# Kernel tuning notes

Hardware: AMD Instinct MI355X
Metric: run time of the kernel (lower is better)

## Reference

```python
import jax, jax.numpy as jnp
import numpy as np

NP, NC, E, EL = 50000, 5000, 200000, 100000
DP, DC, HID, OUT, HEADS = 1280, 256, 128, 128, 4


def setup_inputs() -> dict:
    key = jax.random.key(0)
    ks = jax.random.split(key, 40)
    p = lambda k, shp: jax.random.normal(k, shp, dtype=jnp.float32) * 0.05
    inp = {
        "x_protein": jax.random.normal(ks[0], (NP, DP), dtype=jnp.float32),
        "x_class": jax.random.normal(ks[1], (NC, DC), dtype=jnp.float32),
        "src": jax.random.randint(ks[2], (E,), 0, NP),
        "dst": jax.random.randint(ks[3], (E,), 0, NC),
        "edge_label_src": jax.random.randint(ks[4], (EL,), 0, NP),
        "edge_label_dst": jax.random.randint(ks[5], (EL,), 0, NC),
        # SAGEConv, relation protein->class (updates class nodes)
        "sage_pc_Wl": p(ks[6], (DP, HID)), "sage_pc_bl": p(ks[7], (HID,)), "sage_pc_Wr": p(ks[8], (DC, HID)),
        # SAGEConv, relation class->protein (updates protein nodes)
        "sage_cp_Wl": p(ks[9], (DC, HID)), "sage_cp_bl": p(ks[10], (HID,)), "sage_cp_Wr": p(ks[11], (DP, HID)),
        # GATConv p->c (inputs are hidden after conv1)
        "gat_pc_Wsrc": p(ks[12], (HID, HEADS * HID)), "gat_pc_Wdst": p(ks[13], (HID, HEADS * HID)),
        "gat_pc_asrc": p(ks[14], (HEADS, HID)), "gat_pc_adst": p(ks[15], (HEADS, HID)), "gat_pc_b": p(ks[16], (HID,)),
        # GATConv c->p
        "gat_cp_Wsrc": p(ks[17], (HID, HEADS * HID)), "gat_cp_Wdst": p(ks[18], (HID, HEADS * HID)),
        "gat_cp_asrc": p(ks[19], (HEADS, HID)), "gat_cp_adst": p(ks[20], (HEADS, HID)), "gat_cp_b": p(ks[21], (HID,)),
        # final per-node-type Linear (to_hetero duplicates lin per node type)
        "lin_p_W": p(ks[22], (HID, OUT)), "lin_p_b": p(ks[23], (OUT,)),
        "lin_c_W": p(ks[24], (HID, OUT)), "lin_c_b": p(ks[25], (OUT,)),
        # link predictor
        "link_W": p(ks[26], (2 * OUT, 1)), "link_b": p(ks[27], (1,)),
    }
    return inp


def _sage(x_src, x_dst, s, d, Wl, bl, Wr, n_dst):
    # PyG SAGEConv: lin_l(mean_aggr(x_src)) + lin_r(x_dst); lin_l has bias.
    agg = jax.ops.segment_sum(x_src[s], d, num_segments=n_dst)
    cnt = jax.ops.segment_sum(jnp.ones((s.shape[0], 1), x_src.dtype), d, num_segments=n_dst)
    mean = agg / jnp.maximum(cnt, 1.0)
    return mean @ Wl + bl + x_dst @ Wr


def _gat(x_src, x_dst, s, d, Ws, Wd, a_s, a_d, b, n_dst):
    # PyG GATConv bipartite, heads=HEADS, concat=False, add_self_loops=False.
    H, C = a_s.shape
    hs = (x_src @ Ws).reshape(-1, H, C)   # [Ns, H, C]
    hd = (x_dst @ Wd).reshape(-1, H, C)   # [Nd, H, C]
    als = jnp.einsum('nhc,hc->nh', hs, a_s)
    ald = jnp.einsum('nhc,hc->nh', hd, a_d)
    e = jax.nn.leaky_relu(als[s] + ald[d], 0.2)                    # [E, H]
    emax = jax.ops.segment_max(e, d, num_segments=n_dst)          # stable softmax per dst
    ee = jnp.exp(e - emax[d])
    denom = jax.ops.segment_sum(ee, d, num_segments=n_dst)
    alpha = ee / denom[d]                                          # [E, H]
    out = jax.ops.segment_sum(alpha[:, :, None] * hs[s], d, num_segments=n_dst)  # [Nd, H, C]
    return out.mean(axis=1) + b  # concat=False -> mean over heads


def reference(x_protein, x_class, src, dst, edge_label_src, edge_label_dst,
              sage_pc_Wl, sage_pc_bl, sage_pc_Wr,
              sage_cp_Wl, sage_cp_bl, sage_cp_Wr,
              gat_pc_Wsrc, gat_pc_Wdst, gat_pc_asrc, gat_pc_adst, gat_pc_b,
              gat_cp_Wsrc, gat_cp_Wdst, gat_cp_asrc, gat_cp_adst, gat_cp_b,
              lin_p_W, lin_p_b, lin_c_W, lin_c_b, link_W, link_b):
    # Layer 1: hetero SAGE (each node type has exactly one incoming relation)
    h_c = jax.nn.relu(_sage(x_protein, x_class, src, dst, sage_pc_Wl, sage_pc_bl, sage_pc_Wr, NC))
    h_p = jax.nn.relu(_sage(x_class, x_protein, dst, src, sage_cp_Wl, sage_cp_bl, sage_cp_Wr, NP))
    # Layer 2: hetero GAT
    g_c = jax.nn.relu(_gat(h_p, h_c, src, dst, gat_pc_Wsrc, gat_pc_Wdst, gat_pc_asrc, gat_pc_adst, gat_pc_b, NC))
    g_p = jax.nn.relu(_gat(h_c, h_p, dst, src, gat_cp_Wsrc, gat_cp_Wdst, gat_cp_asrc, gat_cp_adst, gat_cp_b, NP))
    # Per-type output projection
    z_p = g_p @ lin_p_W + lin_p_b
    z_c = g_c @ lin_c_W + lin_c_b
    # Link predictor: gather, concat, linear, sigmoid
    ef = jnp.concatenate([z_p[edge_label_src], z_c[edge_label_dst]], axis=-1)  # [EL, 2*OUT]
    return jax.nn.sigmoid(ef @ link_W + link_b).squeeze(-1)
```

## Files before the change

kernel.cpp:

```cpp
#include <hip/hip_runtime.h>
#include <math.h>

#define NPROT 50000
#define NCLS  5000
#define DIMP  1280
#define DIMC  256
#define SCAN_N (NCLS + NPROT)
#define KSTEPS (DIMP/32)

#define P1B  ((NPROT+127)/128)
#define C1BY ((NCLS+63)/64)
#define C1B  (4*C1BY)

typedef float4 f4;
typedef __attribute__((ext_vector_type(8))) short short8;
typedef __attribute__((ext_vector_type(4))) float f32x4;

__device__ __forceinline__ unsigned short f2bf(float f){
    unsigned u = __float_as_uint(f);
    u += 0x7FFFu + ((u >> 16) & 1u);
    return (unsigned short)(u >> 16);
}
__device__ __forceinline__ float bf2f(unsigned short b){
    return __uint_as_float(((unsigned)b) << 16);
}
__device__ __forceinline__ void gload_lds16(const void* g, void* l){
    __builtin_amdgcn_global_load_lds((const __attribute__((address_space(1))) void*)g,
                                     (__attribute__((address_space(3))) void*)l, 16, 0, 0);
}
__device__ __forceinline__ int OFFV(const int* __restrict__ offv, const int* __restrict__ part, int v){
    return offv[v] + part[v>>10];
}

__global__ __launch_bounds__(512) void mega1(const float* __restrict__ Af,
                                             const unsigned short* __restrict__ BtP,
                                             unsigned short* __restrict__ P1,
                                             const float* __restrict__ Ac,
                                             const float* __restrict__ WcatC,
                                             unsigned short* __restrict__ C1,
                                             const int* __restrict__ src, const int* __restrict__ dst,
                                             const int* __restrict__ offv, const int* __restrict__ part,
                                             int* __restrict__ cur, int* __restrict__ adj, int E){
    __shared__ __align__(16) unsigned char smem[48*1024];
    const int blk = blockIdx.x;
    const int tid = threadIdx.x;

    if(blk < P1B){
        unsigned char* As = smem;
        unsigned char* Bs = smem + 16*1024;
        const int lane = tid & 63;
        const int w    = tid >> 6;
        const int wm   = w >> 2, wn = w & 3;
        const int row0 = blk * 128;
        const int kg = lane >> 4, fr = lane & 15;

        const int ar_  = tid >> 2;
        const int acc_ = tid & 3;
        const int asrow = min(row0 + ar_, NPROT-1);
        const float* aG = Af + (size_t)asrow*DIMP + acc_*8;
        const int awoff = ar_*64 + ((acc_ ^ ((ar_>>1)&3)) << 4);

        f32x4 acc[4][4] = {};
        f4 va, vb;

        auto STAGEB = [&](int buf, int k0){
            #pragma unroll
            for(int i=0;i<2;i++){
                int c  = i*512 + tid;
                int r  = c >> 2, cc = c & 3;
                int scc = cc ^ ((r>>1) & 3);
                gload_lds16((const void*)(BtP + (size_t)r*DIMP + k0 + scc*8),
                            (void*)(Bs + buf*16384 + (i*512 + tid)*16));
            }
        };
        auto WRITEA = [&](int buf){
            union { short8 s; unsigned short u[8]; } uu;
            uu.u[0]=f2bf(va.x); uu.u[1]=f2bf(va.y); uu.u[2]=f2bf(va.z); uu.u[3]=f2bf(va.w);
            uu.u[4]=f2bf(vb.x); uu.u[5]=f2bf(vb.y); uu.u[6]=f2bf(vb.z); uu.u[7]=f2bf(vb.w);
            *(short8*)(As + buf*8192 + awoff) = uu.s;
        };

        STAGEB(0, 0);
        va = *(const f4*)(aG + 0);
        vb = *(const f4*)(aG + 4);
        WRITEA(0);
        va = *(const f4*)(aG + 32);
        vb = *(const f4*)(aG + 36);
        asm volatile("s_waitcnt lgkmcnt(0)" ::: "memory");
        __builtin_amdgcn_sched_barrier(0);

        for(int t=0; t<KSTEPS; ++t){
            __builtin_amdgcn_s_barrier();
            __builtin_amdgcn_sched_barrier(0);

            if(t+1 < KSTEPS){
                WRITEA((t+1)&1);
                STAGEB((t+1)&1, (t+1)*32);
            }
            __builtin_amdgcn_sched_barrier(0);
            if(t+2 < KSTEPS){
                va = *(const f4*)(aG + (t+2)*32);
                vb = *(const f4*)(aG + (t+2)*32 + 4);
            }

            const unsigned char* Ab = As + (t&1)*8192;
            const unsigned char* Bb = Bs + (t&1)*16384;
            short8 aF[4], bF[4];
            #pragma unroll
            for(int m=0;m<4;m++){
                int r = wm*64 + m*16 + fr;
                aF[m] = *(const short8*)(Ab + r*64 + ((kg ^ ((r>>1)&3))<<4));
            }
            #pragma unroll
            for(int n=0;n<4;n++){
                int r = wn*64 + n*16 + fr;
                bF[n] = *(const short8*)(Bb + r*64 + ((kg ^ ((r>>1)&3))<<4));
            }
            #pragma unroll
            for(int m=0;m<4;m++)
            #pragma unroll
            for(int n=0;n<4;n++)
                acc[m][n] = __builtin_amdgcn_mfma_f32_16x16x32_bf16(aF[m], bF[n], acc[m][n], 0, 0, 0);

            if(t+2 < KSTEPS)      asm volatile("s_waitcnt vmcnt(2) lgkmcnt(0)" ::: "memory");
            else                  asm volatile("s_waitcnt vmcnt(0) lgkmcnt(0)" ::: "memory");
            __builtin_amdgcn_sched_barrier(0);
        }

        #pragma unroll
        for(int m=0;m<4;m++)
        #pragma unroll
        for(int r=0;r<4;r++){
            int row = row0 + wm*64 + m*16 + kg*4 + r;
            if(row < NPROT){
                #pragma unroll
                for(int n=0;n<4;n++)
                    P1[(size_t)row*256 + wn*64 + n*16 + fr] = f2bf(acc[m][n][r]);
            }
        }
    } else if(blk < P1B + C1B){
        float (*As64)[68] = (float(*)[68])smem;
        float (*Bs64)[64] = (float(*)[64])(smem + 16*68*4);
        const int bi = blk - P1B;
        const int row0 = (bi >> 2) * 64;
        const int col0 = (bi & 3) * 64;
        const bool act = tid < 256;
        const int ty = tid >> 4;
        const int tx = tid & 15;
        const int m  = tid >> 2;
        const int kq = (tid & 3) << 2;
        const int kb = tid >> 4;
        const int c4 = (tid & 15) << 2;

        float acc[4][4];
        #pragma unroll
        for(int i=0;i<4;i++)
        #pragma unroll
            for(int j=0;j<4;j++) acc[i][j]=0.f;

        const bool arow_ok = act && (row0 + m) < NCLS;
        const float* Abase = Ac + (size_t)(row0 + min(m,255)) * DIMC + kq;
        const float* Bbase = WcatC + col0 + c4 + (size_t)min(kb,15) * 256;

        for(int k0 = 0; k0 < DIMC; k0 += 16){
            if(act){
                f4 av;
                if(arow_ok) av = *(const f4*)(Abase + k0);
                else        av = make_float4(0.f,0.f,0.f,0.f);
                As64[kq+0][m]=av.x; As64[kq+1][m]=av.y; As64[kq+2][m]=av.z; As64[kq+3][m]=av.w;
                *(f4*)&Bs64[kb][c4] = *(const f4*)(Bbase + (size_t)k0 * 256);
            }
            __syncthreads();
            if(act){
                #pragma unroll
                for(int kk=0;kk<16;kk++){
                    f4 a = *(const f4*)&As64[kk][ty<<2];
                    f4 b = *(const f4*)&Bs64[kk][tx<<2];
                    float ar[4]={a.x,a.y,a.z,a.w};
                    float br[4]={b.x,b.y,b.z,b.w};
                    #pragma unroll
                    for(int i=0;i<4;i++)
                    #pragma unroll
                        for(int j=0;j<4;j++) acc[i][j] += ar[i]*br[j];
                }
            }
            __syncthreads();
        }
        if(act){
            #pragma unroll
            for(int i=0;i<4;i++){
                int r = row0 + (ty<<2) + i;
                if(r < NCLS){
                    ushort4 v;
                    v.x=f2bf(acc[i][0]); v.y=f2bf(acc[i][1]);
                    v.z=f2bf(acc[i][2]); v.w=f2bf(acc[i][3]);
                    *(ushort4*)&C1[(size_t)r*256 + col0 + (tx<<2)] = v;
                }
            }
        }
    } else {
        int e = (blk - P1B - C1B)*512 + tid;
        if(e < E){
            int s = src[e], d = dst[e];
            int pc = atomicAdd(&cur[d],1);        adj[OFFV(offv,part,d)+pc] = s;
            int pp = atomicAdd(&cur[NCLS+s],1);   adj[OFFV(offv,part,NCLS+s)+pp] = d;
        }
    }
}

#define NPB ((NPROT+127)/128)
#define NCB ((NCLS+127)/128)
__global__ __launch_bounds__(256) void gemm_hs(const unsigned short* __restrict__ Ap,
                                               const unsigned short* __restrict__ Ac,
                                               const unsigned short* __restrict__ Btp,
                                               const unsigned short* __restrict__ Btc,
                                               const float* __restrict__ projP,
                                               const float* __restrict__ projC,
                                               unsigned short* __restrict__ Cp,
                                               unsigned short* __restrict__ Cc,
                                               float* __restrict__ attP,
                                               float* __restrict__ attC){
    const bool cls = (int)blockIdx.y >= NPB;
    const unsigned short* A  = cls ? Ac : Ap;
    const unsigned short* Bt = cls ? Btc : Btp;
    unsigned short* C = cls ? Cc : Cp;
    const int M = cls ? NCLS : NPROT;
    const int row0 = (cls ? blockIdx.y - NPB : blockIdx.y) * 128;
    const int col0 = blockIdx.x * 128;

    __shared__ __align__(16) unsigned char As[128*32*2];
    __shared__ __align__(16) unsigned char Bs[128*32*2];
    __shared__ float projS[1024];
    const int tid  = threadIdx.x;
    const int lane = tid & 63;
    const int w    = tid >> 6;
    const int wm   = w >> 1, wn = w & 1;
    const int kg = lane >> 4, fr = lane & 15;

    f32x4 acc[4][4] = {};

    for(int k0 = 0; k0 < 128; k0 += 32){
        #pragma unroll
        for(int i=0;i<2;i++){
            int c  = i*256 + w*64 + lane;
            int r  = c >> 2, cc = c & 3;
            int scc = cc ^ ((r>>1) & 3);
            int srow = min(row0 + r, M-1);
            gload_lds16((const void*)(A + (size_t)srow*128 + k0 + scc*8),
                        (void*)(As + (i*256 + w*64)*16));
        }
        #pragma unroll
        for(int i=0;i<2;i++){
            int c  = i*256 + w*64 + lane;
            int r  = c >> 2, cc = c & 3;
            int scc = cc ^ ((r>>1) & 3);
            gload_lds16((const void*)(Bt + (size_t)(col0 + r)*128 + k0 + scc*8),
                        (void*)(Bs + (i*256 + w*64)*16));
        }
        __syncthreads();

        short8 aF[4], bF[4];
        #pragma unroll
        for(int m=0;m<4;m++){
            int r = wm*64 + m*16 + fr;
            int b0 = (r*64 + kg*16) ^ (((r>>1)&3)<<4);
            aF[m] = *(const short8*)(As + b0);
        }
        #pragma unroll
        for(int n=0;n<4;n++){
            int r = wn*64 + n*16 + fr;
            int b0 = (r*64 + kg*16) ^ (((r>>1)&3)<<4);
            bF[n] = *(const short8*)(Bs + b0);
        }
        #pragma unroll
        for(int m=0;m<4;m++)
        #pragma unroll
        for(int n=0;n<4;n++)
            acc[m][n] = __builtin_amdgcn_mfma_f32_16x16x32_bf16(aF[m], bF[n], acc[m][n], 0, 0, 0);
        __syncthreads();
    }

    #pragma unroll
    for(int m=0;m<4;m++)
    #pragma unroll
    for(int r=0;r<4;r++){
        int row = row0 + wm*64 + m*16 + kg*4 + r;
        if(row < M){
            #pragma unroll
            for(int n=0;n<4;n++)
                C[(size_t)row*512 + col0 + wn*64 + n*16 + fr] = f2bf(acc[m][n][r]);
        }
    }

    if(blockIdx.x == 0){
        const float* proj = cls ? projC : projP;
        float* att = cls ? attC : attP;
        for(int i=tid;i<1024;i+=256) projS[i] = proj[i];
        __syncthreads();
        int ri = tid >> 1, cb = (tid & 1)*4;
        int row = row0 + ri;
        if(row < M){
            const unsigned short* ar = A + (size_t)row*128;
            float s0=0.f,s1=0.f,s2=0.f,s3=0.f;
            #pragma unroll
            for(int kk=0;kk<16;kk++){
                short8 a8 = *(const short8*)(ar + kk*8);
                #pragma unroll
                for(int q=0;q<8;q++){
                    float av = bf2f((unsigned short)a8[q]);
                    const float* pr = &projS[(kk*8+q)*8 + cb];
                    s0 += av*pr[0]; s1 += av*pr[1]; s2 += av*pr[2]; s3 += av*pr[3];
                }
            }
            f4 o = make_float4(s0,s1,s2,s3);
            *(f4*)&att[(size_t)row*8 + cb] = o;
        }
    }
}

__global__ void setup(const float* __restrict__ Wl_pc, const float* __restrict__ Wr_cp,
                      const float* __restrict__ Wl_cp, const float* __restrict__ Wr_pc,
                      const float* __restrict__ pcWs, const float* __restrict__ pcAs,
                      const float* __restrict__ pcWd, const float* __restrict__ pcAd,
                      const float* __restrict__ cpWs, const float* __restrict__ cpAs,
                      const float* __restrict__ cpWd, const float* __restrict__ cpAd,
                      const float* __restrict__ lpW, const float* __restrict__ lpb,
                      const float* __restrict__ lcW, const float* __restrict__ lcb,
                      const float* __restrict__ linkW,
                      const int* __restrict__ src, const int* __restrict__ dst,
                      unsigned short* __restrict__ BtP, float* __restrict__ WcatC,
                      unsigned short* __restrict__ BtSp, unsigned short* __restrict__ BtSc,
                      float* __restrict__ projP, float* __restrict__ projC,
                      float* __restrict__ w_p, float* __restrict__ w_c,
                      float* __restrict__ cpc,
                      int* __restrict__ deg, int E){
    int blk = blockIdx.x, tid = threadIdx.x;
    if(blk < 2048){
        int t = blk*256 + tid;
        if(t < 327680){
            int n = t / 1280, k = t % 1280;
            float v = (n<128) ? Wl_pc[(size_t)k*128+n] : Wr_cp[(size_t)k*128+n-128];
            BtP[t] = f2bf(v);
        } else if(t < 393216){
            int i = t - 327680; int k = i>>8, j = i&255;
            WcatC[i] = (j<128) ? Wl_cp[(size_t)k*128+j] : Wr_pc[(size_t)k*128+j-128];
        } else if(t < 458752){
            int i = t - 393216; int n = i>>7, k = i&127;
            BtSp[i] = f2bf(pcWs[(size_t)k*512+n]);
        } else {
            int i = t - 458752; int n = i>>7, k = i&127;
            BtSc[i] = f2bf(cpWs[(size_t)k*512+n]);
        }
    } else if(blk < 2056){
        int sec = (blk-2048) >> 1;
        int t = ((blk-2048) & 1)*256 + tid;
        const float *W, *a; float* proj; int colbase;
        if(sec==0){ W=pcWs; a=pcAs; proj=projP; colbase=0; }
        else if(sec==1){ W=cpWd; a=cpAd; proj=projP; colbase=4; }
        else if(sec==2){ W=pcWd; a=pcAd; proj=projC; colbase=0; }
        else { W=cpWs; a=cpAs; proj=projC; colbase=4; }
        int k = t >> 2, h = t & 3;
        const float* w = W + (size_t)k*512 + h*128;
        const float* av = a + h*128;
        float s=0.f;
        for(int c=0;c<128;c++) s += w[c]*av[c];
        proj[k*8 + colbase + h] = s;
    } else if(blk == 2056){
        if(tid < 128){
            float s=0.f;
            for(int o=0;o<128;o++) s += lpW[(size_t)tid*128+o]*linkW[o];
            w_p[tid]=s;
        } else {
            int j=tid-128;
            float s=0.f;
            for(int o=0;o<128;o++) s += lcW[(size_t)j*128+o]*linkW[128+o];
            w_c[j]=s;
        }
        if(tid==0){ float s=0.f; for(int o=0;o<128;o++) s+=lpb[o]*linkW[o];      cpc[0]=s; }
        if(tid==1){ float s=0.f; for(int o=0;o<128;o++) s+=lcb[o]*linkW[128+o];  cpc[1]=s; }
    } else {
        int e = (blk-2057)*256 + tid;
        if(e < E){
            atomicAdd(&deg[dst[e]],1);
            atomicAdd(&deg[NCLS + src[e]],1);
        }
    }
}

__global__ __launch_bounds__(1024) void scan1(const int* __restrict__ in, int* __restrict__ out,
                                              int* __restrict__ part, int n){
    __shared__ int buf[1024];
    int tid = threadIdx.x;
    int g = blockIdx.x*1024 + tid;
    int v = (g<n) ? in[g] : 0;
    buf[tid] = v;
    __syncthreads();
    for(int o=1;o<1024;o<<=1){
        int t = (tid>=o) ? buf[tid-o] : 0;
        __syncthreads();
        buf[tid] += t;
        __syncthreads();
    }
    if(g<n) out[g] = buf[tid] - v;
    if(tid==1023) part[blockIdx.x] = buf[1023];
}
__global__ __launch_bounds__(64) void scan2(int* __restrict__ part, int nb,
                                            int* __restrict__ offv, int n){
    int tid = threadIdx.x;
    int orig = (tid<nb) ? part[tid] : 0;
    int v = orig;
    #pragma unroll
    for(int o=1;o<64;o<<=1){
        int t = __shfl_up(v, o);
        if(tid>=o) v += t;
    }
    int total = __shfl(v, nb-1);
    if(tid<nb) part[tid] = v - orig;
    if(tid == (n>>10)) offv[n] = total - (v - orig);
}

__global__ __launch_bounds__(256) void sage_all(const int* __restrict__ offv, const int* __restrict__ part,
                                                const int* __restrict__ adj,
                                                const unsigned short* __restrict__ P1,
                                                const unsigned short* __restrict__ C1,
                                                const float* __restrict__ bl_pc, const float* __restrict__ bl_cp,
                                                unsigned short* __restrict__ h_c, unsigned short* __restrict__ h_p){
    int v = blockIdx.x*4 + (threadIdx.x>>6);
    int l = threadIdx.x & 63;
    if(v >= SCAN_N) return;
    int b = OFFV(offv,part,v), deg = OFFV(offv,part,v+1)-b;
    float a0=0.f, a1=0.f;
    float inv = 1.f/(float)max(deg,1);
    if(v < NCLS){
        #pragma unroll 4
        for(int i=0;i<deg;i++){
            int s = adj[b+i];
            ushort2 w = *((const ushort2*)P1 + (size_t)s*128 + l);
            a0 += bf2f(w.x); a1 += bf2f(w.y);
        }
        ushort2 sv = *((const ushort2*)C1 + (size_t)v*128 + 64 + l);
        float h0 = fmaxf(a0*inv + bl_pc[2*l]   + bf2f(sv.x), 0.f);
        float h1 = fmaxf(a1*inv + bl_pc[2*l+1] + bf2f(sv.y), 0.f);
        ushort2 o; o.x=f2bf(h0); o.y=f2bf(h1);
        *((ushort2*)h_c + (size_t)v*64 + l) = o;
    } else {
        int m = v - NCLS;
        #pragma unroll 4
        for(int i=0;i<deg;i++){
            int d = adj[b+i];
            ushort2 w = *((const ushort2*)C1 + (size_t)d*128 + l);
            a0 += bf2f(w.x); a1 += bf2f(w.y);
        }
        ushort2 sv = *((const ushort2*)P1 + (size_t)m*128 + 64 + l);
        float h0 = fmaxf(a0*inv + bl_cp[2*l]   + bf2f(sv.x), 0.f);
        float h1 = fmaxf(a1*inv + bl_cp[2*l+1] + bf2f(sv.y), 0.f);
        ushort2 o; o.x=f2bf(h0); o.y=f2bf(h1);
        *((ushort2*)h_p + (size_t)m*64 + l) = o;
    }
}

__global__ __launch_bounds__(128) void gat_all(const int* __restrict__ offv, const int* __restrict__ part,
                                               const int* __restrict__ adj,
                                               const float* __restrict__ attP, const float* __restrict__ attC,
                                               const unsigned short* __restrict__ hs_p,
                                               const unsigned short* __restrict__ hs_c,
                                               const float* __restrict__ gb_pc, const float* __restrict__ gb_cp,
                                               const float* __restrict__ w_c, const float* __restrict__ w_p,
                                               const float* __restrict__ cpc,
                                               float* __restrict__ u_c, float* __restrict__ u_p){
    __shared__ float ald[4];
    __shared__ int   adjS[32];
    __shared__ float eeS[32*4];
    __shared__ float den8[8];
    __shared__ f4    red4[32];

    int n = blockIdx.x;
    const bool cls = n < NCLS;
    const int node = cls ? n : n - NCLS;
    const float* attS = cls ? attP : attC;
    const float* attD = cls ? attC : attP;
    const int abase = cls ? 0 : 4;
    const unsigned short* hs = cls ? hs_p : hs_c;
    const float* gb = cls ? gb_pc : gb_cp;
    const float* wv = cls ? w_c : w_p;
    float* u = cls ? u_c : u_p;
    const int cidx = cls ? 1 : 0;

    int j = threadIdx.x;
    const int hh = j >> 5;
    const int q  = j & 31;
    int b = OFFV(offv,part,n), deg = OFFV(offv,part,n+1)-b;
    if(j < 4) ald[j] = attD[(size_t)node*8 + abase + j];

    float a0=0.f, a1=0.f, a2=0.f, a3=0.f;
    float denP = 0.f;

    for(int base=0; base<deg; base+=32){
        int cnt = min(32, deg-base);
        if(j < cnt) adjS[j] = adj[b+base+j];
        __syncthreads();
        if(j < cnt*4){
            int i = j>>2, h = j&3;
            int s = adjS[i];
            float e = attS[(size_t)s*8 + abase + h] + ald[h];
            e = e > 0.f ? e : 0.2f*e;
            float ee = __expf(e);
            eeS[j] = ee;
            denP += ee;
        }
        __syncthreads();
        #pragma unroll 4
        for(int ii=0; ii<cnt; ii++){
            int s = adjS[ii];
            float ee = eeS[ii*4 + hh];
            ushort4 v = *(const ushort4*)(hs + (size_t)s*512 + hh*128 + q*4);
            a0 += ee*bf2f(v.x); a1 += ee*bf2f(v.y);
            a2 += ee*bf2f(v.z); a3 += ee*bf2f(v.w);
        }
        __syncthreads();
    }

    float dp = denP;
    dp += __shfl_xor(dp, 4);
    dp += __shfl_xor(dp, 8);
    dp += __shfl_xor(dp, 16);
    dp += __shfl_xor(dp, 32);
    if((j & 63) < 4) den8[(j>>6)*4 + (j&3)] = dp;
    __syncthreads();

    float den_h = den8[hh] + den8[4+hh];
    float inv = (deg > 0) ? 0.25f/den_h : 0.f;
    a0 *= inv; a1 *= inv; a2 *= inv; a3 *= inv;

    a0 += __shfl_xor(a0, 32); a1 += __shfl_xor(a1, 32);
    a2 += __shfl_xor(a2, 32); a3 += __shfl_xor(a3, 32);
    if(j >= 64 && j < 96) red4[q] = make_float4(a0,a1,a2,a3);
    __syncthreads();
    float val = 0.f;
    if(j < 32){
        f4 r = red4[q];
        float t0 = a0 + r.x, t1 = a1 + r.y, t2 = a2 + r.z, t3 = a3 + r.w;
        const float* gbq = gb + q*4;
        const float* wvq = wv + q*4;
        val = fmaxf(t0 + gbq[0], 0.f)*wvq[0]
            + fmaxf(t1 + gbq[1], 0.f)*wvq[1]
            + fmaxf(t2 + gbq[2], 0.f)*wvq[2]
            + fmaxf(t3 + gbq[3], 0.f)*wvq[3];
    }
    #pragma unroll
    for(int o=16;o;o>>=1) val += __shfl_down(val, o);
    if(j == 0) u[node] = val + cpc[cidx];
}

__global__ void link_out(const int* __restrict__ els, const int* __restrict__ eld,
                         const float* __restrict__ u_p, const float* __restrict__ u_c,
                         const float* __restrict__ linkb, float* __restrict__ out, int EL){
    int i = blockIdx.x*256 + threadIdx.x;
    if(i >= EL) return;
    float x = u_p[els[i]] + u_c[eld[i]] + linkb[0];
    out[i] = 1.f/(1.f + __expf(-x));
}

extern "C" void kernel_launch(void* const* d_in, const int* in_sizes, int n_in,
                              void* d_out, int out_size, void* d_ws, size_t ws_size,
                              hipStream_t stream){
    const float* x_p  = (const float*)d_in[0];
    const float* x_c  = (const float*)d_in[1];
    const int*   src  = (const int*)d_in[2];
    const int*   dst  = (const int*)d_in[3];
    const int*   els  = (const int*)d_in[4];
    const int*   eld  = (const int*)d_in[5];
    const float* sage_pc_Wl = (const float*)d_in[6];
    const float* sage_pc_bl = (const float*)d_in[7];
    const float* sage_pc_Wr = (const float*)d_in[8];
    const float* sage_cp_Wl = (const float*)d_in[9];
    const float* sage_cp_bl = (const float*)d_in[10];
    const float* sage_cp_Wr = (const float*)d_in[11];
    const float* gat_pc_Wsrc = (const float*)d_in[12];
    const float* gat_pc_Wdst = (const float*)d_in[13];
    const float* gat_pc_asrc = (const float*)d_in[14];
    const float* gat_pc_adst = (const float*)d_in[15];
    const float* gat_pc_b    = (const float*)d_in[16];
    const float* gat_cp_Wsrc = (const float*)d_in[17];
    const float* gat_cp_Wdst = (const float*)d_in[18];
    const float* gat_cp_asrc = (const float*)d_in[19];
    const float* gat_cp_adst = (const float*)d_in[20];
    const float* gat_cp_b    = (const float*)d_in[21];
    const float* lin_p_W = (const float*)d_in[22];
    const float* lin_p_b = (const float*)d_in[23];
    const float* lin_c_W = (const float*)d_in[24];
    const float* lin_c_b = (const float*)d_in[25];
    const float* link_W  = (const float*)d_in[26];
    const float* link_b  = (const float*)d_in[27];

    const int E  = in_sizes[2];
    const int EL = in_sizes[4];

    float* ws = (float*)d_ws;
    size_t off = 0;
    auto alloc = [&](size_t n)->float*{ float* p = ws + off; off += (n + 3) & ~(size_t)3; return p; };

    unsigned short* BtP  = (unsigned short*)alloc((size_t)256*DIMP/2);
    float* WcatC = alloc((size_t)DIMC*256);
    unsigned short* BtSp = (unsigned short*)alloc((size_t)512*128/2);
    unsigned short* BtSc = (unsigned short*)alloc((size_t)512*128/2);
    unsigned short* P1   = (unsigned short*)alloc((size_t)NPROT*256/2);
    unsigned short* C1   = (unsigned short*)alloc((size_t)NCLS*256/2);
    unsigned short* h_p  = (unsigned short*)alloc((size_t)NPROT*128/2);
    unsigned short* h_c  = (unsigned short*)alloc((size_t)NCLS*128/2);
    unsigned short* hs_p = (unsigned short*)alloc((size_t)NPROT*512/2);
    unsigned short* hs_c = (unsigned short*)alloc((size_t)NCLS*512/2);
    float* attP  = alloc((size_t)NPROT*8);
    float* attC  = alloc((size_t)NCLS*8);
    float* projP = alloc(128*8);
    float* projC = alloc(128*8);
    float* w_p   = alloc(128);
    float* w_c   = alloc(128);
    float* cpc   = alloc(4);
    int* degcur = (int*)alloc((size_t)2*SCAN_N);
    int* deg = degcur;
    int* cur = degcur + SCAN_N;
    int* offv = (int*)alloc(SCAN_N+1);
    int* part = (int*)alloc(64);
    int* adj  = (int*)alloc((size_t)2*E);
    float* u_p = alloc(NPROT);
    float* u_c = alloc(NCLS);
    if(off*4 > ws_size) return;

    hipMemsetAsync(degcur, 0, (size_t)2*SCAN_N*4, stream);

    setup<<<2057 + (E+255)/256, 256, 0, stream>>>(
        sage_pc_Wl, sage_cp_Wr, sage_cp_Wl, sage_pc_Wr,
        gat_pc_Wsrc, gat_pc_asrc, gat_pc_Wdst, gat_pc_adst,
        gat_cp_Wsrc, gat_cp_asrc, gat_cp_Wdst, gat_cp_adst,
        lin_p_W, lin_p_b, lin_c_W, lin_c_b, link_W,
        src, dst,
        BtP, WcatC, BtSp, BtSc, projP, projC, w_p, w_c, cpc, deg, E);

    const int NB = (SCAN_N + 1023)/1024;
    scan1<<<NB,1024,0,stream>>>(deg, offv, part, SCAN_N);
    scan2<<<1,64,0,stream>>>(part, NB, offv, SCAN_N);

    const int FILLB = (E+511)/512;
    mega1<<<P1B + C1B + FILLB, 512, 0, stream>>>(x_p, BtP, P1, x_c, WcatC, C1,
                                                 src, dst, offv, part, cur, adj, E);

    sage_all<<<(SCAN_N+3)/4,256,0,stream>>>(offv, part, adj, P1, C1, sage_pc_bl, sage_cp_bl, h_c, h_p);

    gemm_hs<<<dim3(4,NPB+NCB),256,0,stream>>>(h_p, h_c, BtSp, BtSc, projP, projC,
                                              hs_p, hs_c, attP, attC);

    gat_all<<<SCAN_N,128,0,stream>>>(offv, part, adj, attP, attC, hs_p, hs_c,
                                     gat_pc_b, gat_cp_b, w_c, w_p, cpc, u_c, u_p);

    link_out<<<(EL+255)/256,256,0,stream>>>(els, eld, u_p, u_c, link_b, (float*)d_out, EL);
}
```

Before: 315.7 us.

## Use one wavefront per node in GAT, reorder mega1 blocks, simplify GEMM pipeline

```diff
diff --git a/kernel.cpp b/kernel.cpp
--- a/kernel.cpp
+++ b/kernel.cpp
@@ -44,104 +44,12 @@
     __shared__ __align__(16) unsigned char smem[48*1024];
     const int blk = blockIdx.x;
     const int tid = threadIdx.x;
-
-    if(blk < P1B){
-        unsigned char* As = smem;
-        unsigned char* Bs = smem + 16*1024;
-        const int lane = tid & 63;
-        const int w    = tid >> 6;
-        const int wm   = w >> 2, wn = w & 3;
-        const int row0 = blk * 128;
-        const int kg = lane >> 4, fr = lane & 15;
-
-        const int ar_  = tid >> 2;
-        const int acc_ = tid & 3;
-        const int asrow = min(row0 + ar_, NPROT-1);
-        const float* aG = Af + (size_t)asrow*DIMP + acc_*8;
-        const int awoff = ar_*64 + ((acc_ ^ ((ar_>>1)&3)) << 4);
-
-        f32x4 acc[4][4] = {};
-        f4 va, vb;
-
-        auto STAGEB = [&](int buf, int k0){
-            #pragma unroll
-            for(int i=0;i<2;i++){
-                int c  = i*512 + tid;
-                int r  = c >> 2, cc = c & 3;
-                int scc = cc ^ ((r>>1) & 3);
-                gload_lds16((const void*)(BtP + (size_t)r*DIMP + k0 + scc*8),
-                            (void*)(Bs + buf*16384 + (i*512 + tid)*16));
-            }
-        };
-        auto WRITEA = [&](int buf){
-            union { short8 s; unsigned short u[8]; } uu;
-            uu.u[0]=f2bf(va.x); uu.u[1]=f2bf(va.y); uu.u[2]=f2bf(va.z); uu.u[3]=f2bf(va.w);
-            uu.u[4]=f2bf(vb.x); uu.u[5]=f2bf(vb.y); uu.u[6]=f2bf(vb.z); uu.u[7]=f2bf(vb.w);
-            *(short8*)(As + buf*8192 + awoff) = uu.s;
-        };
-
-        STAGEB(0, 0);
-        va = *(const f4*)(aG + 0);
-        vb = *(const f4*)(aG + 4);
-        WRITEA(0);
-        va = *(const f4*)(aG + 32);
-        vb = *(const f4*)(aG + 36);
-        asm volatile("s_waitcnt lgkmcnt(0)" ::: "memory");
-        __builtin_amdgcn_sched_barrier(0);
-
-        for(int t=0; t<KSTEPS; ++t){
-            __builtin_amdgcn_s_barrier();
-            __builtin_amdgcn_sched_barrier(0);
-
-            if(t+1 < KSTEPS){
-                WRITEA((t+1)&1);
-                STAGEB((t+1)&1, (t+1)*32);
-            }
-            __builtin_amdgcn_sched_barrier(0);
-            if(t+2 < KSTEPS){
-                va = *(const f4*)(aG + (t+2)*32);
-                vb = *(const f4*)(aG + (t+2)*32 + 4);
-            }
-
-            const unsigned char* Ab = As + (t&1)*8192;
-            const unsigned char* Bb = Bs + (t&1)*16384;
-            short8 aF[4], bF[4];
-            #pragma unroll
-            for(int m=0;m<4;m++){
-                int r = wm*64 + m*16 + fr;
-                aF[m] = *(const short8*)(Ab + r*64 + ((kg ^ ((r>>1)&3))<<4));
-            }
-            #pragma unroll
-            for(int n=0;n<4;n++){
-                int r = wn*64 + n*16 + fr;
-                bF[n] = *(const short8*)(Bb + r*64 + ((kg ^ ((r>>1)&3))<<4));
-            }
-            #pragma unroll
-            for(int m=0;m<4;m++)
-            #pragma unroll
-            for(int n=0;n<4;n++)
-                acc[m][n] = __builtin_amdgcn_mfma_f32_16x16x32_bf16(aF[m], bF[n], acc[m][n], 0, 0, 0);
-
-            if(t+2 < KSTEPS)      asm volatile("s_waitcnt vmcnt(2) lgkmcnt(0)" ::: "memory");
-            else                  asm volatile("s_waitcnt vmcnt(0) lgkmcnt(0)" ::: "memory");
-            __builtin_amdgcn_sched_barrier(0);
-        }
-
-        #pragma unroll
-        for(int m=0;m<4;m++)
-        #pragma unroll
-        for(int r=0;r<4;r++){
-            int row = row0 + wm*64 + m*16 + kg*4 + r;
-            if(row < NPROT){
-                #pragma unroll
-                for(int n=0;n<4;n++)
-                    P1[(size_t)row*256 + wn*64 + n*16 + fr] = f2bf(acc[m][n][r]);
-            }
-        }
-    } else if(blk < P1B + C1B){
+    const int FILLB = (E + 511) / 512;
+
+    if(blk < C1B){
         float (*As64)[68] = (float(*)[68])smem;
         float (*Bs64)[64] = (float(*)[64])(smem + 16*68*4);
-        const int bi = blk - P1B;
+        const int bi = blk;
         const int row0 = (bi >> 2) * 64;
         const int col0 = (bi & 3) * 64;
         const bool act = tid < 256;
@@ -198,12 +106,96 @@
                 }
             }
         }
-    } else {
-        int e = (blk - P1B - C1B)*512 + tid;
+    } else if(blk < C1B + FILLB){
+        int e = (blk - C1B)*512 + tid;
         if(e < E){
             int s = src[e], d = dst[e];
             int pc = atomicAdd(&cur[d],1);        adj[OFFV(offv,part,d)+pc] = s;
             int pp = atomicAdd(&cur[NCLS+s],1);   adj[OFFV(offv,part,NCLS+s)+pp] = d;
+        }
+    } else {
+        const int pblk = blk - C1B - FILLB;
+        unsigned char* As = smem;
+        unsigned char* Bs = smem + 16*1024;
+        const int lane = tid & 63;
+        const int w    = tid >> 6;
+        const int wm   = w >> 2, wn = w & 3;
+        const int row0 = pblk * 128;
+        const int kg = lane >> 4, fr = lane & 15;
+
+        const int ar_  = tid >> 2;
+        const int acc_ = tid & 3;
+        const int asrow = min(row0 + ar_, NPROT-1);
+        const float* aG = Af + (size_t)asrow*DIMP + acc_*8;
+        const int awoff = ar_*64 + ((acc_ ^ ((ar_>>1)&3)) << 4);
+
+        f32x4 acc[4][4] = {};
+        f4 va, vb;
+
+        auto STAGEB = [&](int buf, int k0){
+            #pragma unroll
+            for(int i=0;i<2;i++){
+                int c  = i*512 + tid;
+                int r  = c >> 2, cc = c & 3;
+                int scc = cc ^ ((r>>1) & 3);
+                gload_lds16((const void*)(BtP + (size_t)r*DIMP + k0 + scc*8),
+                            (void*)(Bs + buf*16384 + (i*512 + tid)*16));
+            }
+        };
+        auto WRITEA = [&](int buf){
+            union { short8 s; unsigned short u[8]; } uu;
+            uu.u[0]=f2bf(va.x); uu.u[1]=f2bf(va.y); uu.u[2]=f2bf(va.z); uu.u[3]=f2bf(va.w);
+            uu.u[4]=f2bf(vb.x); uu.u[5]=f2bf(vb.y); uu.u[6]=f2bf(vb.z); uu.u[7]=f2bf(vb.w);
+            *(short8*)(As + buf*8192 + awoff) = uu.s;
+        };
+
+        va = *(const f4*)(aG + 0);
+        vb = *(const f4*)(aG + 4);
+        STAGEB(0, 0);
+        WRITEA(0);
+        __syncthreads();
+
+        for(int t=0; t<KSTEPS; ++t){
+            const int cb = t & 1;
+            if(t+1 < KSTEPS){
+                va = *(const f4*)(aG + (t+1)*32);
+                vb = *(const f4*)(aG + (t+1)*32 + 4);
+                STAGEB(cb^1, (t+1)*32);
+            }
+
+            const unsigned char* Ab = As + cb*8192;
+            const unsigned char* Bb = Bs + cb*16384;
+            short8 aF[4], bF[4];
+            #pragma unroll
+            for(int m=0;m<4;m++){
+                int r = wm*64 + m*16 + fr;
+                aF[m] = *(const short8*)(Ab + r*64 + ((kg ^ ((r>>1)&3))<<4));
+            }
+            #pragma unroll
+            for(int n=0;n<4;n++){
+                int r = wn*64 + n*16 + fr;
+                bF[n] = *(const short8*)(Bb + r*64 + ((kg ^ ((r>>1)&3))<<4));
+            }
+            #pragma unroll
+            for(int m=0;m<4;m++)
+            #pragma unroll
+            for(int n=0;n<4;n++)
+                acc[m][n] = __builtin_amdgcn_mfma_f32_16x16x32_bf16(aF[m], bF[n], acc[m][n], 0, 0, 0);
+
+            if(t+1 < KSTEPS) WRITEA(cb^1);
+            __syncthreads();
+        }
+
+        #pragma unroll
+        for(int m=0;m<4;m++)
+        #pragma unroll
+        for(int r=0;r<4;r++){
+            int row = row0 + wm*64 + m*16 + kg*4 + r;
+            if(row < NPROT){
+                #pragma unroll
+                for(int n=0;n<4;n++)
+                    P1[(size_t)row*256 + wn*64 + n*16 + fr] = f2bf(acc[m][n][r]);
+            }
         }
     }
 }
@@ -459,7 +451,7 @@
     }
 }
 
-__global__ __launch_bounds__(128) void gat_all(const int* __restrict__ offv, const int* __restrict__ part,
+__global__ __launch_bounds__(512) void gat_all(const int* __restrict__ offv, const int* __restrict__ part,
                                                const int* __restrict__ adj,
                                                const float* __restrict__ attP, const float* __restrict__ attC,
                                                const unsigned short* __restrict__ hs_p,
@@ -468,13 +460,9 @@
                                                const float* __restrict__ w_c, const float* __restrict__ w_p,
                                                const float* __restrict__ cpc,
                                                float* __restrict__ u_c, float* __restrict__ u_p){
-    __shared__ float ald[4];
-    __shared__ int   adjS[32];
-    __shared__ float eeS[32*4];
-    __shared__ float den8[8];
-    __shared__ f4    red4[32];
-
-    int n = blockIdx.x;
+    int n = blockIdx.x*8 + (threadIdx.x>>6);
+    if(n >= SCAN_N) return;
+    const int lane = threadIdx.x & 63;
     const bool cls = n < NCLS;
     const int node = cls ? n : n - NCLS;
     const float* attS = cls ? attP : attC;
@@ -486,70 +474,45 @@
     float* u = cls ? u_c : u_p;
     const int cidx = cls ? 1 : 0;
 
-    int j = threadIdx.x;
-    const int hh = j >> 5;
-    const int q  = j & 31;
+    const int h  = lane >> 4;
+    const int c8 = lane & 15;
     int b = OFFV(offv,part,n), deg = OFFV(offv,part,n+1)-b;
-    if(j < 4) ald[j] = attD[(size_t)node*8 + abase + j];
-
-    float a0=0.f, a1=0.f, a2=0.f, a3=0.f;
-    float denP = 0.f;
-
-    for(int base=0; base<deg; base+=32){
-        int cnt = min(32, deg-base);
-        if(j < cnt) adjS[j] = adj[b+base+j];
-        __syncthreads();
-        if(j < cnt*4){
-            int i = j>>2, h = j&3;
-            int s = adjS[i];
-            float e = attS[(size_t)s*8 + abase + h] + ald[h];
-            e = e > 0.f ? e : 0.2f*e;
-            float ee = __expf(e);
-            eeS[j] = ee;
-            denP += ee;
-        }
-        __syncthreads();
-        #pragma unroll 4
-        for(int ii=0; ii<cnt; ii++){
-            int s = adjS[ii];
-            float ee = eeS[ii*4 + hh];
-            ushort4 v = *(const ushort4*)(hs + (size_t)s*512 + hh*128 + q*4);
-            a0 += ee*bf2f(v.x); a1 += ee*bf2f(v.y);
-            a2 += ee*bf2f(v.z); a3 += ee*bf2f(v.w);
-        }
-        __syncthreads();
-    }
-
-    float dp = denP;
-    dp += __shfl_xor(dp, 4);
-    dp += __shfl_xor(dp, 8);
-    dp += __shfl_xor(dp, 16);
-    dp += __shfl_xor(dp, 32);
-    if((j & 63) < 4) den8[(j>>6)*4 + (j&3)] = dp;
-    __syncthreads();
-
-    float den_h = den8[hh] + den8[4+hh];
-    float inv = (deg > 0) ? 0.25f/den_h : 0.f;
-    a0 *= inv; a1 *= inv; a2 *= inv; a3 *= inv;
-
-    a0 += __shfl_xor(a0, 32); a1 += __shfl_xor(a1, 32);
-    a2 += __shfl_xor(a2, 32); a3 += __shfl_xor(a3, 32);
-    if(j >= 64 && j < 96) red4[q] = make_float4(a0,a1,a2,a3);
-    __syncthreads();
+    const float ald_h = attD[(size_t)node*8 + abase + h];
+
+    float acc[8] = {};
+    float den = 0.f;
+
+    for(int ii=0; ii<deg; ++ii){
+        int s = __builtin_amdgcn_readfirstlane(adj[b+ii]);
+        float e = attS[(size_t)s*8 + abase + h] + ald_h;
+        e = e > 0.f ? e : 0.2f*e;
+        float ee = __expf(e);
+        den += ee;
+        short8 v8 = *(const short8*)(hs + (size_t)s*512 + h*128 + c8*8);
+        #pragma unroll
+        for(int q=0;q<8;q++) acc[q] += ee * bf2f((unsigned short)v8[q]);
+    }
+
+    float inv = (deg > 0) ? 0.25f/den : 0.f;
+    #pragma unroll
+    for(int q=0;q<8;q++){
+        float x = acc[q]*inv;
+        x += __shfl_xor(x, 16);
+        x += __shfl_xor(x, 32);
+        acc[q] = x;
+    }
+
     float val = 0.f;
-    if(j < 32){
-        f4 r = red4[q];
-        float t0 = a0 + r.x, t1 = a1 + r.y, t2 = a2 + r.z, t3 = a3 + r.w;
-        const float* gbq = gb + q*4;
-        const float* wvq = wv + q*4;
-        val = fmaxf(t0 + gbq[0], 0.f)*wvq[0]
-            + fmaxf(t1 + gbq[1], 0.f)*wvq[1]
-            + fmaxf(t2 + gbq[2], 0.f)*wvq[2]
-            + fmaxf(t3 + gbq[3], 0.f)*wvq[3];
-    }
     #pragma unroll
-    for(int o=16;o;o>>=1) val += __shfl_down(val, o);
-    if(j == 0) u[node] = val + cpc[cidx];
+    for(int q=0;q<8;q++){
+        int c = c8*8 + q;
+        val += fmaxf(acc[q] + gb[c], 0.f) * wv[c];
+    }
+    val += __shfl_xor(val, 1);
+    val += __shfl_xor(val, 2);
+    val += __shfl_xor(val, 4);
+    val += __shfl_xor(val, 8);
+    if(lane == 0) u[node] = val + cpc[cidx];
 }
 
 __global__ void link_out(const int* __restrict__ els, const int* __restrict__ eld,
@@ -642,7 +605,7 @@
     scan2<<<1,64,0,stream>>>(part, NB, offv, SCAN_N);
 
     const int FILLB = (E+511)/512;
-    mega1<<<P1B + C1B + FILLB, 512, 0, stream>>>(x_p, BtP, P1, x_c, WcatC, C1,
+    mega1<<<C1B + FILLB + P1B, 512, 0, stream>>>(x_p, BtP, P1, x_c, WcatC, C1,
                                                  src, dst, offv, part, cur, adj, E);
 
     sage_all<<<(SCAN_N+3)/4,256,0,stream>>>(offv, part, adj, P1, C1, sage_pc_bl, sage_cp_bl, h_c, h_p);
@@ -650,8 +613,8 @@
     gemm_hs<<<dim3(4,NPB+NCB),256,0,stream>>>(h_p, h_c, BtSp, BtSc, projP, projC,
                                               hs_p, hs_c, attP, attC);
 
-    gat_all<<<SCAN_N,128,0,stream>>>(offv, part, adj, attP, attC, hs_p, hs_c,
-                                     gat_pc_b, gat_cp_b, w_c, w_p, cpc, u_c, u_p);
+    gat_all<<<(SCAN_N+7)/8,512,0,stream>>>(offv, part, adj, attP, attC, hs_p, hs_c,
+                                           gat_pc_b, gat_cp_b, w_c, w_p, cpc, u_c, u_p);
 
     link_out<<<(EL+255)/256,256,0,stream>>>(els, eld, u_p, u_c, link_b, (float*)d_out, EL);
 }
```

Measured after the change: 289.0 us (median of 2 runs). 1.09x faster.
